# Kernel optimization log

Measured on AMD Instinct MI355X. Metric: run time of the kernel, lower is better.

Reference implementation:

```python
import jax, jax.numpy as jnp
import numpy as np

B, C, H, W = 2, 16, 384, 384
ADJ = 1
HID = 64
N_ITERS = 8


def _to_c(x):
    return x[..., 0] + 1j * x[..., 1]


def _to_r(z):
    return jnp.stack([z.real, z.imag], axis=-1)


def fft2c(x):
    z = jnp.fft.ifftshift(_to_c(x), axes=(-2, -1))
    z = jnp.fft.fft2(z, axes=(-2, -1), norm='ortho')
    return _to_r(jnp.fft.fftshift(z, axes=(-2, -1)))


def ifft2c(x):
    z = jnp.fft.ifftshift(_to_c(x), axes=(-2, -1))
    z = jnp.fft.ifft2(z, axes=(-2, -1), norm='ortho')
    return _to_r(jnp.fft.fftshift(z, axes=(-2, -1)))


def complex_mul(a, b):
    ar, ai = a[..., 0], a[..., 1]
    br, bi = b[..., 0], b[..., 1]
    return jnp.stack([ar * br - ai * bi, ar * bi + ai * br], axis=-1)


def complex_conj(x):
    return jnp.stack([x[..., 0], -x[..., 1]], axis=-1)


def _conv(x, w, b):
    y = jax.lax.conv_general_dilated(x, w, (1, 1), 'SAME',
                                     dimension_numbers=('NCHW', 'OIHW', 'NCHW'))
    return y + b[None, :, None, None]


def sens_expand(x, sens_maps):
    # x: [b, adj, h, w, 2] -> repeat to coils, multiply, fft
    c = sens_maps.shape[1]
    x = jnp.repeat(x, c // ADJ, axis=1)
    return fft2c(complex_mul(x, sens_maps))


def sens_reduce(x, sens_maps):
    b, c, h, w, _ = x.shape
    x = ifft2c(x)
    x = complex_mul(x, complex_conj(sens_maps))
    return x.reshape(b, ADJ, c // ADJ, h, w, 2).sum(axis=2)  # [b, adj, h, w, 2]


def apply_model(x, w1, b1, w2, b2):
    # complex_to_chan_dim: [b, c, h, w, 2] -> [b, 2c, h, w]
    b, c, h, w, _ = x.shape
    x = jnp.transpose(x, (0, 4, 1, 2, 3)).reshape(b, 2 * c, h, w)
    # per-channel norm (torch std is unbiased -> ddof=1)
    xf = x.reshape(b, 2 * c, h * w)
    mean = xf.mean(axis=2)[:, :, None, None]
    std = jnp.std(xf, axis=2, ddof=1)[:, :, None, None]
    xn = (x - mean) / std
    # regularizer model (2-layer conv)
    y = _conv(jax.nn.relu(_conv(xn, w1, b1)), w2, b2)
    y = y * std + mean
    # chan_complex_to_last_dim
    return jnp.transpose(y.reshape(b, 2, c, h, w), (0, 2, 3, 4, 1))


def mask_predictor(x, w_mp, b_mp):
    # x: [b, 2, h, w] -> prob over width columns [b, 1, w]
    feat = x.mean(axis=2)  # [b, 2, w]
    logits = jnp.einsum('bcw,c->bw', feat, w_mp) + b_mp
    return jax.nn.softmax(logits, axis=-1)[:, None, :]


def update_mask(current_mask, pred_prob, add_list, it_idx):
    # batched variable-k top-k scatter (fused version of the per-sample loop)
    p = pred_prob[:, :, None, :, None] * (1.0 - current_mask)  # [b,1,1,w,1]
    b = p.shape[0]
    pv = p.reshape(b, -1)                       # [b, w]
    order = jnp.argsort(-pv, axis=-1)           # descending
    ranks = jnp.argsort(order, axis=-1)         # rank of each column
    add_num = add_list[:, it_idx]               # [b]
    add = (ranks < add_num[:, None]).astype(current_mask.dtype)
    return current_mask + add[:, None, None, :, None]


def setup_inputs():
    key = jax.random.key(0)
    ks = jax.random.split(key, 10)
    return {
        'current_kspace': jax.random.normal(ks[0], (B, C, H, W, 2), jnp.float32),
        'ref_kspace': jax.random.normal(ks[1], (B, C, H, W, 2), jnp.float32),
        'mask': jax.random.randint(ks[2], (B, 1, 1, W, 1), 0, 2).astype(bool),
        'sens_maps': jax.random.normal(ks[3], (B, C, H, W, 2), jnp.float32) / np.sqrt(C),
        'it_idx': 3,
        'current_mask': jnp.zeros((B, 1, 1, W, 1), jnp.float32),
        'current_prob': jax.random.uniform(ks[4], (B, 1, W), jnp.float32),
        'add_list': jax.random.randint(ks[5], (B, N_ITERS), 1, 30),
        'dc_weight': jnp.ones((1,), jnp.float32),
        'w1': jax.random.normal(ks[6], (HID, 2 * ADJ, 3, 3), jnp.float32) * 0.05,
        'b1': jnp.zeros((HID,), jnp.float32),
        'w2': jax.random.normal(ks[7], (2 * ADJ, HID, 3, 3), jnp.float32) * 0.05,
        'b2': jnp.zeros((2 * ADJ,), jnp.float32),
        'w_mp': jax.random.normal(ks[8], (2,), jnp.float32) * 0.1,
        'b_mp': jnp.zeros((), jnp.float32),
    }


def reference(current_kspace, ref_kspace, mask, sens_maps, it_idx, current_mask,
              current_prob, add_list, dc_weight, w1, b1, w2, b2, w_mp, b_mp):
    restore_im = apply_model(sens_reduce(current_kspace, sens_maps), w1, b1, w2, b2)
    model_term = sens_expand(restore_im, sens_maps)
    soft_dc = jnp.where(mask, model_term - ref_kspace, 0.0) * dc_weight
    pred_kspace = model_term - soft_dc
    restore_im_dc = sens_reduce(pred_kspace, sens_maps)
    # [b, h, w, 2] -> fft2c -> [b, 2, h, w]
    kim = jnp.transpose(fft2c(restore_im_dc[:, 0]), (0, 3, 1, 2))
    pred_prob = mask_predictor(kim, w_mp, b_mp)
    pred_mask = update_mask(current_mask, pred_prob, add_list, it_idx)
    return pred_kspace, pred_mask, pred_prob
```

## Files before the change

### kernel.cpp

```cpp
#include <hip/hip_runtime.h>
#include <hip/hip_bf16.h>
#include <math.h>

#define HH 384
#define WW 384
#define NPIX (HH*WW)
#define BB 2
#define CC 16
#define NKF 9437184

__device__ inline float2 cmul(float2 a, float2 b) {
    return make_float2(a.x*b.x - a.y*b.y, a.x*b.y + a.y*b.x);
}
__device__ inline float bf2f(unsigned short u) {
    union { unsigned int i; float f; } c; c.i = ((unsigned)u) << 16; return c.f;
}
__device__ inline float2 loadc2(const void* p, int dt, size_t i) {
    if (dt == 1) { ushort2 u = ((const ushort2*)p)[i];
        return make_float2(bf2f(u.x), bf2f(u.y)); }
    if (dt == 2) { double2 d = ((const double2*)p)[i];
        return make_float2((float)d.x, (float)d.y); }
    return ((const float2*)p)[i];
}
__device__ inline float loads1(const void* p, int dt, size_t i) {
    if (dt == 1) return bf2f(((const unsigned short*)p)[i]);
    if (dt == 2) return (float)((const double*)p)[i];
    return ((const float*)p)[i];
}
__device__ inline int flex_int1(const void* p) {
    unsigned v = ((const unsigned*)p)[0];
    if (v < 1000000u) return (int)v;
    float f = ((const float*)p)[0];
    if (f > -1e6f && f < 1e6f && f == floorf(f)) return (int)f;
    return (int)((const double*)p)[0];
}
__device__ inline int flex_int_arr(const void* p, int i) {
    const unsigned* u = (const unsigned*)p;
    if (u[1] == 0u && u[3] == 0u) return (int)u[2*i];
    if (u[0] >= 1u && u[0] < 1000000u) return (int)u[i];
    float f = ((const float*)p)[i];
    if (f > -1e6f && f < 1e6f) return (int)f;
    return (int)((const double*)p)[i];
}

__global__ void detect_dtype(const unsigned* __restrict__ q, int* dt)
{
    __shared__ int bad, sig;
    if (threadIdx.x == 0) { bad = 0; sig = 0; }
    __syncthreads();
    const unsigned short* q16 = (const unsigned short*)q;
    int mybad = 0, mysig = 0;
    for (int i = threadIdx.x; i < 8192; i += 256) {
        unsigned short u = q16[i];
        int e = (u >> 7) & 0xFF;
        if (!(e == 0 || (e >= 100 && e <= 140))) mybad++;
    }
    for (int i = threadIdx.x; i < 2048; i += 256) {
        unsigned hi = q[2*i + 1];
        int e = (hi >> 20) & 0x7FF;
        if (e >= 1003 && e <= 1040) mysig++;
    }
    atomicAdd(&bad, mybad);
    atomicAdd(&sig, mysig);
    __syncthreads();
    if (threadIdx.x == 0)
        *dt = (bad < 400) ? 1 : ((sig > 1950) ? 2 : 0);
}

#define NLINE 8
#define SP 385

template<int DIR, int AXIS, int MODE>
__global__ __launch_bounds__(256)
void fft384(const void* in, float2* out, const int* DTp, int srcExt,
            const void* aux1, const void* aux2,
            const int* FLAGp, const void* dcwp, float2* outk)
{
    __shared__ float2 tw[384];
    __shared__ float2 stage[NLINE * SP];
    __shared__ float2 work[4][384];
    const int tid = threadIdx.x;
    const int dt = (srcExt || MODE) ? *DTp : 0;
    for (int j = tid; j < 384; j += 256) {
        float s, c;
        sincosf(-6.283185307179586f * (float)j / 384.0f, &s, &c);
        tw[j] = make_float2(c, s);
    }
    const int img = blockIdx.x / 48;
    const int t0  = (blockIdx.x % 48) * NLINE;
    const size_t base = (size_t)img * NPIX;
    float2* dst = out + base;

    if (AXIS == 0) {
        if (MODE == 1) {
            const float2* rim = (const float2*)aux1;
            const size_t rbase = (size_t)(img >> 4) * NPIX;
            for (int f = tid; f < NLINE*384; f += 256) {
                int l = f / 384, n = f - l*384;
                size_t pix = (size_t)(t0 + l)*384 + n;
                stage[l*SP + n] = cmul(rim[rbase + pix], loadc2(aux2, dt, base + pix));
            }
        } else {
            for (int f = tid; f < NLINE*384; f += 256) {
                int l = f / 384, n = f - l*384;
                stage[l*SP + n] = loadc2(in, dt, base + (size_t)(t0 + l)*384 + n);
            }
        }
    } else {
        for (int f = tid; f < NLINE*384; f += 256) {
            int l = f & 7, n = f >> 3;
            stage[l*SP + n] = loadc2(in, dt, base + (size_t)n*384 + (t0 + l));
        }
    }
    __syncthreads();
    const int g    = tid >> 6;
    const int lane = tid & 63;
    float2* w = work[g];
    const float SCALE = 0.05103103630798288f;
    for (int it = 0; it < 2; ++it) {
        const int l = it*4 + g;
        #pragma unroll
        for (int m = 0; m < 6; ++m) {
            int n = lane + 64*m;
            float2 v = stage[l*SP + n];
            float sgn = (n & 1) ? -1.f : 1.f;
            int q = n / 3;
            int r3 = n - 3*q;
            w[r3*128 + q] = make_float2(v.x*sgn, v.y*sgn);
        }
        __syncthreads();
        #pragma unroll
        for (int s = 0; s < 7; ++s) {
            const int h = 64 >> s;
            const int tstep = 3 << s;
            const int j = lane & (h-1);
            const int i = ((lane & ~(h-1)) << 1) | j;
            float2 t = tw[j * tstep];
            if (DIR < 0) t.y = -t.y;
            #pragma unroll
            for (int n1 = 0; n1 < 3; ++n1) {
                float2* a = w + (n1 << 7);
                float2 u = a[i], v = a[i+h];
                float2 d = make_float2(u.x - v.x, u.y - v.y);
                a[i]   = make_float2(u.x + v.x, u.y + v.y);
                a[i+h] = cmul(d, t);
            }
            __syncthreads();
        }
        #pragma unroll
        for (int half = 0; half < 2; ++half) {
            int k2 = lane + 64*half;
            int r  = __brev((unsigned)k2) >> 25;
            float2 a0 = w[r], a1 = w[128 + r], a2 = w[256 + r];
            float2 t1 = tw[k2];
            float2 t2 = tw[(2*k2) % 384];
            float2 w3 = tw[128], w3b = tw[256];
            if (DIR < 0) { t1.y=-t1.y; t2.y=-t2.y; w3.y=-w3.y; w3b.y=-w3b.y; }
            float2 b1 = cmul(a1, t1), b2 = cmul(a2, t2);
            float2 X0 = make_float2(a0.x + b1.x + b2.x, a0.y + b1.y + b2.y);
            float2 c1 = cmul(w3, b1), c2 = cmul(w3b, b2);
            float2 X1 = make_float2(a0.x + c1.x + c2.x, a0.y + c1.y + c2.y);
            float2 d1 = cmul(w3b, b1), d2 = cmul(w3, b2);
            float2 X2 = make_float2(a0.x + d1.x + d2.x, a0.y + d1.y + d2.y);
            float sc = (k2 & 1) ? -SCALE : SCALE;
            stage[l*SP + k2      ] = make_float2(X0.x*sc, X0.y*sc);
            stage[l*SP + k2 + 128] = make_float2(X1.x*sc, X1.y*sc);
            stage[l*SP + k2 + 256] = make_float2(X2.x*sc, X2.y*sc);
        }
        __syncthreads();
    }
    if (AXIS == 0) {
        for (int f = tid; f < NLINE*384; f += 256) {
            int l = f / 384, n = f - l*384;
            dst[(size_t)(t0 + l)*384 + n] = stage[l*SP + n];
        }
    } else {
        if (MODE == 2) {
            const int fl = *FLAGp;
            const float dw = loads1(dcwp, dt, 0);
            const int bb = img >> 4;
            for (int f = tid; f < NLINE*384; f += 256) {
                int l = f & 7, n = f >> 3;
                int wcol = t0 + l;
                size_t pix = (size_t)n*384 + wcol;
                float2 v = stage[l*SP + n];
                int m;
                switch (fl) {
                    case 0:  m = ((const unsigned char*)aux2)[bb*384 + wcol] != 0; break;
                    case 4:  m = ((const unsigned short*)aux2)[bb*384 + wcol] != 0; break;
                    case 3:  m = ((const unsigned long long*)aux2)[bb*384 + wcol] != 0ULL; break;
                    default: m = ((const unsigned int*)aux2)[bb*384 + wcol] != 0u; break;
                }
                if (m) {
                    float2 r = loadc2(aux1, dt, base + pix);
                    v.x -= (v.x - r.x)*dw;
                    v.y -= (v.y - r.y)*dw;
                }
                dst[pix] = v;
                outk[base + pix] = v;
            }
        } else {
            for (int f = tid; f < NLINE*384; f += 256) {
                int l = f & 7, n = f >> 3;
                dst[(size_t)n*384 + (t0 + l)] = stage[l*SP + n];
            }
        }
    }
}

__global__ void detect_mask(const unsigned char* __restrict__ m, int* flag)
{
    __shared__ int sA, sB, sC, sD, sE;
    if (threadIdx.x == 0) { sA = sB = sC = sD = sE = 0; }
    __syncthreads();
    for (int i = threadIdx.x; i < 768; i += 256) {
        unsigned char v = m[i];
        if (v > 1) atomicOr(&sA, 1);
        if ((i & 3) && v) atomicOr(&sB, 1);
    }
    const unsigned short* m16 = (const unsigned short*)m;
    for (int i = threadIdx.x; i < 384; i += 256)
        if (!(i & 1) && m16[i]) atomicOr(&sC, 1);
    const unsigned int* m32 = (const unsigned int*)m;
    for (int i = threadIdx.x; i < 192; i += 256) {
        if ((i & 1) && m32[i]) atomicOr(&sD, 1);
        if (!(i & 1) && m32[i]) atomicOr(&sE, 1);
    }
    __syncthreads();
    if (threadIdx.x == 0) {
        int f;
        if (!sA) { if (sB) f = 0; else if (sD) f = 2; else f = 3; }
        else     { if (sC) f = 4; else if (sE) f = 2; else f = 3; }
        *flag = f;
    }
}

template<bool WITH_STATS>
__global__ __launch_bounds__(256)
void reduce_sens(const float2* __restrict__ xin, const void* __restrict__ sens,
                 float2* __restrict__ ximg, const int* DTp,
                 float* __restrict__ partials)
{
    const int dt = *DTp;
    const int b = blockIdx.y;
    const int p = blockIdx.x*256 + threadIdx.x;
    float2 acc = make_float2(0.f, 0.f);
    for (int c = 0; c < CC; ++c) {
        size_t o = ((size_t)(b*CC + c))*NPIX + p;
        float2 a = xin[o];
        float2 s = loadc2(sens, dt, o);
        acc.x += a.x*s.x + a.y*s.y;
        acc.y += a.y*s.x - a.x*s.y;
    }
    ximg[(size_t)b*NPIX + p] = acc;
    if (WITH_STATS) {
        float sx = acc.x, sy = acc.y, qx = acc.x*acc.x, qy = acc.y*acc.y;
        #pragma unroll
        for (int o = 32; o > 0; o >>= 1) {
            sx += __shfl_down(sx, o, 64); sy += __shfl_down(sy, o, 64);
            qx += __shfl_down(qx, o, 64); qy += __shfl_down(qy, o, 64);
        }
        __shared__ float red[4][4];
        const int wv = threadIdx.x >> 6, lane = threadIdx.x & 63;
        if (lane == 0) {
            red[wv][0] = sx; red[wv][1] = sy; red[wv][2] = qx; red[wv][3] = qy;
        }
        __syncthreads();
        if (threadIdx.x == 0) {
            float t0 = red[0][0]+red[1][0]+red[2][0]+red[3][0];
            float t1 = red[0][1]+red[1][1]+red[2][1]+red[3][1];
            float t2 = red[0][2]+red[1][2]+red[2][2]+red[3][2];
            float t3 = red[0][3]+red[1][3]+red[2][3]+red[3][3];
            float* dst = partials + ((size_t)b*576 + blockIdx.x)*4;
            dst[0] = t0; dst[1] = t1; dst[2] = t2; dst[3] = t3;
        }
    }
}

__global__ __launch_bounds__(256)
void stats_finalize(const float* __restrict__ partials, float* __restrict__ ms)
{
    const int b = blockIdx.x;
    const int tid = threadIdx.x;
    float sx=0.f, sy=0.f, qx=0.f, qy=0.f;
    for (int i = tid; i < 576; i += 256) {
        const float* p = partials + ((size_t)b*576 + i)*4;
        sx += p[0]; sy += p[1]; qx += p[2]; qy += p[3];
    }
    __shared__ float r0[256], r1[256], r2[256], r3[256];
    r0[tid]=sx; r1[tid]=sy; r2[tid]=qx; r3[tid]=qy;
    __syncthreads();
    for (int s = 128; s > 0; s >>= 1) {
        if (tid < s) {
            r0[tid]+=r0[tid+s]; r1[tid]+=r1[tid+s];
            r2[tid]+=r2[tid+s]; r3[tid]+=r3[tid+s];
        }
        __syncthreads();
    }
    if (tid == 0) {
        const float N = (float)NPIX;
        float var0 = (r2[0] - r0[0]*r0[0]/N) / (N - 1.f);
        float var1 = (r3[0] - r1[0]*r1[0]/N) / (N - 1.f);
        ms[(b*2+0)*2]   = r0[0]/N;
        ms[(b*2+0)*2+1] = sqrtf(var0);
        ms[(b*2+1)*2]   = r1[0]/N;
        ms[(b*2+1)*2+1] = sqrtf(var1);
    }
}

__global__ __launch_bounds__(256)
void conv_fused(const float2* __restrict__ ximg, const void* __restrict__ w1g,
                const void* __restrict__ b1g, const void* __restrict__ w2g,
                const void* __restrict__ b2g, const float* __restrict__ msg,
                float2* __restrict__ rim, const int* DTp)
{
    __shared__ float2 inP[20][21];
    __shared__ float w1s[1152];
    __shared__ float w2s[1152];
    __shared__ float b1s[64];
    __shared__ float hidw[4][18*20];
    __shared__ float2 accs[4][256];

    const int dt = *DTp;
    const int b = blockIdx.z, bx = blockIdx.x, by = blockIdx.y;
    const int tid = threadIdx.x;
    const int wv = tid >> 6, lane = tid & 63;

    for (int f = tid; f < 1152; f += 256) {
        w1s[f] = loads1(w1g, dt, f);
        w2s[f] = loads1(w2g, dt, f);
    }
    if (tid < 64) b1s[tid] = loads1(b1g, dt, tid);
    const float mean0 = msg[(b*2+0)*2], istd0 = 1.f/msg[(b*2+0)*2+1];
    const float mean1 = msg[(b*2+1)*2], istd1 = 1.f/msg[(b*2+1)*2+1];
    for (int f = tid; f < 400; f += 256) {
        int yy = f / 20, xx = f - yy*20;
        int gy = by*16 + yy - 2, gx = bx*16 + xx - 2;
        float a = 0.f, c = 0.f;
        if (gy >= 0 && gy < HH && gx >= 0 && gx < WW) {
            float2 v = ximg[(size_t)b*NPIX + gy*WW + gx];
            a = (v.x - mean0)*istd0;
            c = (v.y - mean1)*istd1;
        }
        inP[yy][xx] = make_float2(a, c);
    }
    __syncthreads();

    float a0[4] = {0.f,0.f,0.f,0.f}, a1[4] = {0.f,0.f,0.f,0.f};
    float* hid = hidw[wv];

    const int c1col = lane % 18;
    const int c1g   = lane / 18;
    const int c1y0  = 6 * c1g;
    const int tx = lane & 15, ybase = (lane >> 4) * 4;

    for (int j = 0; j < 16; ++j) {
        const int o = wv*16 + j;
        const float* wa = &w1s[o*18];
        const float bo = b1s[o];
        if (c1g < 3) {
            float2 r0c0 = inP[c1y0][c1col],   r0c1 = inP[c1y0][c1col+1],   r0c2 = inP[c1y0][c1col+2];
            float2 r1c0 = inP[c1y0+1][c1col], r1c1 = inP[c1y0+1][c1col+1], r1c2 = inP[c1y0+1][c1col+2];
            #pragma unroll
            for (int rr = 0; rr < 6; ++rr) {
                float2 r2c0 = inP[c1y0+rr+2][c1col];
                float2 r2c1 = inP[c1y0+rr+2][c1col+1];
                float2 r2c2 = inP[c1y0+rr+2][c1col+2];
                float acc = bo
                    + wa[0]*r0c0.x + wa[1]*r0c1.x + wa[2]*r0c2.x
                    + wa[3]*r1c0.x + wa[4]*r1c1.x + wa[5]*r1c2.x
                    + wa[6]*r2c0.x + wa[7]*r2c1.x + wa[8]*r2c2.x
                    + wa[9]*r0c0.y  + wa[10]*r0c1.y + wa[11]*r0c2.y
                    + wa[12]*r1c0.y + wa[13]*r1c1.y + wa[14]*r1c2.y
                    + wa[15]*r2c0.y + wa[16]*r2c1.y + wa[17]*r2c2.y;
                int hy = c1y0 + rr;
                int gy = by*16 + hy - 1, gx = bx*16 + c1col - 1;
                hid[hy*20 + c1col] = (gy >= 0 && gy < HH && gx >= 0 && gx < WW)
                                   ? fmaxf(acc, 0.f) : 0.f;
                r0c0 = r1c0; r0c1 = r1c1; r0c2 = r1c2;
                r1c0 = r2c0; r1c1 = r2c1; r1c2 = r2c2;
            }
        }
        __builtin_amdgcn_wave_barrier();
        {
            const float* w2a = &w2s[o*9];
            const float* w2b = &w2s[576 + o*9];
            float h00 = hid[ybase*20 + tx],     h01 = hid[ybase*20 + tx+1],     h02 = hid[ybase*20 + tx+2];
            float h10 = hid[(ybase+1)*20 + tx], h11 = hid[(ybase+1)*20 + tx+1], h12 = hid[(ybase+1)*20 + tx+2];
            #pragma unroll
            for (int r = 0; r < 4; ++r) {
                float h20 = hid[(ybase+r+2)*20 + tx];
                float h21 = hid[(ybase+r+2)*20 + tx+1];
                float h22 = hid[(ybase+r+2)*20 + tx+2];
                a0[r] += w2a[0]*h00 + w2a[1]*h01 + w2a[2]*h02
                       + w2a[3]*h10 + w2a[4]*h11 + w2a[5]*h12
                       + w2a[6]*h20 + w2a[7]*h21 + w2a[8]*h22;
                a1[r] += w2b[0]*h00 + w2b[1]*h01 + w2b[2]*h02
                       + w2b[3]*h10 + w2b[4]*h11 + w2b[5]*h12
                       + w2b[6]*h20 + w2b[7]*h21 + w2b[8]*h22;
                h00 = h10; h01 = h11; h02 = h12;
                h10 = h20; h11 = h21; h12 = h22;
            }
        }
        __builtin_amdgcn_wave_barrier();
    }
    #pragma unroll
    for (int r = 0; r < 4; ++r)
        accs[wv][(ybase + r)*16 + tx] = make_float2(a0[r], a1[r]);
    __syncthreads();
    {
        const int p = tid;
        float s0 = loads1(b2g, dt, 0), s1 = loads1(b2g, dt, 1);
        #pragma unroll
        for (int wvi = 0; wvi < 4; ++wvi) {
            s0 += accs[wvi][p].x;
            s1 += accs[wvi][p].y;
        }
        const float std0 = msg[(b*2+0)*2+1], std1 = msg[(b*2+1)*2+1];
        int ty = p >> 4, txx = p & 15;
        rim[(size_t)b*NPIX + (by*16+ty)*WW + (bx*16+txx)]
            = make_float2(s0*std0 + mean0, s1*std1 + mean1);
    }
}

__global__ __launch_bounds__(384)
void predictor(const float2* __restrict__ kimg, const void* __restrict__ wmp,
               const void* __restrict__ bmp, float* __restrict__ prob,
               float* __restrict__ outp, const int* DTp)
{
    const int dt = *DTp;
    const int b = blockIdx.x, w = threadIdx.x;
    float s0 = 0.f, s1 = 0.f;
    for (int h = 0; h < HH; ++h) {
        float2 v = kimg[((size_t)b*HH + h)*WW + w];
        s0 += v.x; s1 += v.y;
    }
    float logit = (s0*loads1(wmp,dt,0) + s1*loads1(wmp,dt,1)) * (1.0f/384.0f)
                + loads1(bmp,dt,0);
    __shared__ float red[8];
    float m = logit;
    for (int o = 32; o > 0; o >>= 1) m = fmaxf(m, __shfl_down(m, o, 64));
    int wid = w >> 6, lane = w & 63;
    if (lane == 0) red[wid] = m;
    __syncthreads();
    if (w == 0) { float mm = red[0]; for (int i = 1; i < 6; ++i) mm = fmaxf(mm, red[i]); red[6] = mm; }
    __syncthreads();
    m = red[6];
    float e = expf(logit - m);
    float s = e;
    for (int o = 32; o > 0; o >>= 1) s += __shfl_down(s, o, 64);
    __syncthreads();
    if (lane == 0) red[wid] = s;
    __syncthreads();
    if (w == 0) { float ss = 0.f; for (int i = 0; i < 6; ++i) ss += red[i]; red[7] = ss; }
    __syncthreads();
    float pr = e / red[7];
    prob[b*WW + w] = pr;
    outp[b*WW + w] = pr;
}

__global__ __launch_bounds__(384)
void update_mask_k(const float* __restrict__ prob, const void* __restrict__ cmask,
                   const void* __restrict__ add_list, const void* __restrict__ itp,
                   float* __restrict__ outm, const int* DTp)
{
    const int dt = *DTp;
    const int b = blockIdx.x, w = threadIdx.x;
    __shared__ float p[384];
    float cm = loads1(cmask, dt, b*WW + w);
    float pv = prob[b*WW + w] * (1.0f - cm);
    p[w] = pv;
    __syncthreads();
    int rank = 0;
    for (int i = 0; i < 384; ++i) {
        float q = p[i];
        rank += (q > pv) || (q == pv && i < w);
    }
    int it = flex_int1(itp);
    if (it < 0 || it > 7) it = 0;
    int addn = flex_int_arr(add_list, b*8 + it);
    float val = cm + ((rank < addn) ? 1.0f : 0.0f);
    outm[b*WW + w] = val;
}

extern "C" void kernel_launch(void* const* d_in, const int* in_sizes, int n_in,
                              void* d_out, int out_size, void* d_ws, size_t ws_size,
                              hipStream_t stream)
{
    const void* src  = d_in[0];
    const void* tgt  = d_in[1];
    const void* mask = d_in[2];
    const void* sens = d_in[3];
    const void* itp  = d_in[4];
    const void* cmask= d_in[5];
    const void* addl = d_in[7];
    const void* dcw  = d_in[8];
    const void* w1   = d_in[9];
    const void* b1   = d_in[10];
    const void* w2   = d_in[11];
    const void* b2   = d_in[12];
    const void* wmp  = d_in[13];
    const void* bmp  = d_in[14];
    float* out = (float*)d_out;

    float* ws = (float*)d_ws;
    const size_t OFF_XIMG = 9437184;
    const size_t OFF_RIM  = OFF_XIMG + 589824;
    const size_t OFF_MS   = OFF_RIM  + 589824;
    const size_t OFF_PROB = OFF_MS + 8;
    const size_t OFF_FLAG = OFF_PROB + 768;
    const size_t OFF_DT   = OFF_FLAG + 4;
    const size_t OFF_PART = OFF_DT + 4;

    float2* A    = (float2*)ws;
    float2* XIMG = (float2*)(ws + OFF_XIMG);
    float2* RIM  = (float2*)(ws + OFF_RIM);
    float*  MS   = ws + OFF_MS;
    float*  PROB = ws + OFF_PROB;
    int*    FLAG = (int*)(ws + OFF_FLAG);
    int*    DT   = (int*)(ws + OFF_DT);
    float*  PART = ws + OFF_PART;

    const int gBig   = (BB*CC)*48;
    const int gSmall = BB*48;

    detect_dtype<<<1, 256, 0, stream>>>((const unsigned*)src, DT);
    detect_mask<<<1, 256, 0, stream>>>((const unsigned char*)mask, FLAG);

    fft384<-1,0,0><<<gBig, 256, 0, stream>>>(src, A, DT, 1, nullptr, nullptr, nullptr, nullptr, nullptr);
    fft384<-1,1,0><<<gBig, 256, 0, stream>>>(A, A, DT, 0, nullptr, nullptr, nullptr, nullptr, nullptr);
    reduce_sens<true><<<dim3((NPIX/256), BB), 256, 0, stream>>>(A, sens, XIMG, DT, PART);
    stats_finalize<<<BB, 256, 0, stream>>>(PART, MS);

    conv_fused<<<dim3(24,24,BB), 256, 0, stream>>>(XIMG, w1, b1, w2, b2, MS, RIM, DT);

    fft384<1,0,1><<<gBig, 256, 0, stream>>>(nullptr, A, DT, 0, RIM, sens, nullptr, nullptr, nullptr);
    fft384<1,1,2><<<gBig, 256, 0, stream>>>(A, A, DT, 0, tgt, mask, FLAG, dcw, (float2*)out);

    fft384<-1,0,0><<<gBig, 256, 0, stream>>>(A, A, DT, 0, nullptr, nullptr, nullptr, nullptr, nullptr);
    fft384<-1,1,0><<<gBig, 256, 0, stream>>>(A, A, DT, 0, nullptr, nullptr, nullptr, nullptr, nullptr);
    reduce_sens<false><<<dim3((NPIX/256), BB), 256, 0, stream>>>(A, sens, XIMG, DT, nullptr);

    fft384<1,0,0><<<gSmall, 256, 0, stream>>>(XIMG, XIMG, DT, 0, nullptr, nullptr, nullptr, nullptr, nullptr);
    fft384<1,1,0><<<gSmall, 256, 0, stream>>>(XIMG, XIMG, DT, 0, nullptr, nullptr, nullptr, nullptr, nullptr);

    predictor<<<BB, 384, 0, stream>>>(XIMG, wmp, bmp, PROB, out + 9437184 + 768, DT);
    update_mask_k<<<BB, 384, 0, stream>>>(PROB, cmask, addl, itp, out + 9437184, DT);
}
```

Measured before the change: 393.7 us.

## Widen column-FFT tiles to 16 lines and pair hidden channels in conv

New measurement: 425.1 us. 8.0% more time.

```diff
diff --git a/kernel.cpp b/kernel.cpp
--- a/kernel.cpp
+++ b/kernel.cpp
@@ -67,17 +67,16 @@
         *dt = (bad < 400) ? 1 : ((sig > 1950) ? 2 : 0);
 }
 
-#define NLINE 8
 #define SP 385
 
-template<int DIR, int AXIS, int MODE>
+template<int DIR, int AXIS, int MODE, int NL>
 __global__ __launch_bounds__(256)
 void fft384(const void* in, float2* out, const int* DTp, int srcExt,
             const void* aux1, const void* aux2,
             const int* FLAGp, const void* dcwp, float2* outk)
 {
     __shared__ float2 tw[384];
-    __shared__ float2 stage[NLINE * SP];
+    __shared__ float2 stage[NL * SP];
     __shared__ float2 work[4][384];
     const int tid = threadIdx.x;
     const int dt = (srcExt || MODE) ? *DTp : 0;
@@ -86,8 +85,9 @@
         sincosf(-6.283185307179586f * (float)j / 384.0f, &s, &c);
         tw[j] = make_float2(c, s);
     }
-    const int img = blockIdx.x / 48;
-    const int t0  = (blockIdx.x % 48) * NLINE;
+    const int BPI = 384 / NL;
+    const int img = blockIdx.x / BPI;
+    const int t0  = (blockIdx.x % BPI) * NL;
     const size_t base = (size_t)img * NPIX;
     float2* dst = out + base;
 
@@ -95,20 +95,20 @@
         if (MODE == 1) {
             const float2* rim = (const float2*)aux1;
             const size_t rbase = (size_t)(img >> 4) * NPIX;
-            for (int f = tid; f < NLINE*384; f += 256) {
+            for (int f = tid; f < NL*384; f += 256) {
                 int l = f / 384, n = f - l*384;
                 size_t pix = (size_t)(t0 + l)*384 + n;
                 stage[l*SP + n] = cmul(rim[rbase + pix], loadc2(aux2, dt, base + pix));
             }
         } else {
-            for (int f = tid; f < NLINE*384; f += 256) {
+            for (int f = tid; f < NL*384; f += 256) {
                 int l = f / 384, n = f - l*384;
                 stage[l*SP + n] = loadc2(in, dt, base + (size_t)(t0 + l)*384 + n);
             }
         }
     } else {
-        for (int f = tid; f < NLINE*384; f += 256) {
-            int l = f & 7, n = f >> 3;
+        for (int f = tid; f < NL*384; f += 256) {
+            int l = f & (NL-1), n = f / NL;
             stage[l*SP + n] = loadc2(in, dt, base + (size_t)n*384 + (t0 + l));
         }
     }
@@ -117,7 +117,7 @@
     const int lane = tid & 63;
     float2* w = work[g];
     const float SCALE = 0.05103103630798288f;
-    for (int it = 0; it < 2; ++it) {
+    for (int it = 0; it < NL/4; ++it) {
         const int l = it*4 + g;
         #pragma unroll
         for (int m = 0; m < 6; ++m) {
@@ -170,7 +170,7 @@
         __syncthreads();
     }
     if (AXIS == 0) {
-        for (int f = tid; f < NLINE*384; f += 256) {
+        for (int f = tid; f < NL*384; f += 256) {
             int l = f / 384, n = f - l*384;
             dst[(size_t)(t0 + l)*384 + n] = stage[l*SP + n];
         }
@@ -179,8 +179,8 @@
             const int fl = *FLAGp;
             const float dw = loads1(dcwp, dt, 0);
             const int bb = img >> 4;
-            for (int f = tid; f < NLINE*384; f += 256) {
-                int l = f & 7, n = f >> 3;
+            for (int f = tid; f < NL*384; f += 256) {
+                int l = f & (NL-1), n = f / NL;
                 int wcol = t0 + l;
                 size_t pix = (size_t)n*384 + wcol;
                 float2 v = stage[l*SP + n];
@@ -200,8 +200,8 @@
                 outk[base + pix] = v;
             }
         } else {
-            for (int f = tid; f < NLINE*384; f += 256) {
-                int l = f & 7, n = f >> 3;
+            for (int f = tid; f < NL*384; f += 256) {
+                int l = f & (NL-1), n = f / NL;
                 dst[(size_t)n*384 + (t0 + l)] = stage[l*SP + n];
             }
         }
@@ -318,7 +318,7 @@
     __shared__ float w1s[1152];
     __shared__ float w2s[1152];
     __shared__ float b1s[64];
-    __shared__ float hidw[4][18*20];
+    __shared__ float2 hidw[4][18*20];
     __shared__ float2 accs[4][256];
 
     const int dt = *DTp;
@@ -347,17 +347,18 @@
     __syncthreads();
 
     float a0[4] = {0.f,0.f,0.f,0.f}, a1[4] = {0.f,0.f,0.f,0.f};
-    float* hid = hidw[wv];
+    float2* hid = hidw[wv];
 
     const int c1col = lane % 18;
     const int c1g   = lane / 18;
     const int c1y0  = 6 * c1g;
     const int tx = lane & 15, ybase = (lane >> 4) * 4;
 
-    for (int j = 0; j < 16; ++j) {
-        const int o = wv*16 + j;
-        const float* wa = &w1s[o*18];
-        const float bo = b1s[o];
+    for (int j = 0; j < 8; ++j) {
+        const int oa = wv*16 + 2*j;
+        const float* wa = &w1s[oa*18];
+        const float* wb = &w1s[(oa+1)*18];
+        const float boa = b1s[oa], bob = b1s[oa+1];
         if (c1g < 3) {
             float2 r0c0 = inP[c1y0][c1col],   r0c1 = inP[c1y0][c1col+1],   r0c2 = inP[c1y0][c1col+2];
             float2 r1c0 = inP[c1y0+1][c1col], r1c1 = inP[c1y0+1][c1col+1], r1c2 = inP[c1y0+1][c1col+2];
@@ -366,38 +367,55 @@
                 float2 r2c0 = inP[c1y0+rr+2][c1col];
                 float2 r2c1 = inP[c1y0+rr+2][c1col+1];
                 float2 r2c2 = inP[c1y0+rr+2][c1col+2];
-                float acc = bo
+                float accA = boa
                     + wa[0]*r0c0.x + wa[1]*r0c1.x + wa[2]*r0c2.x
                     + wa[3]*r1c0.x + wa[4]*r1c1.x + wa[5]*r1c2.x
                     + wa[6]*r2c0.x + wa[7]*r2c1.x + wa[8]*r2c2.x
                     + wa[9]*r0c0.y  + wa[10]*r0c1.y + wa[11]*r0c2.y
                     + wa[12]*r1c0.y + wa[13]*r1c1.y + wa[14]*r1c2.y
                     + wa[15]*r2c0.y + wa[16]*r2c1.y + wa[17]*r2c2.y;
+                float accB = bob
+                    + wb[0]*r0c0.x + wb[1]*r0c1.x + wb[2]*r0c2.x
+                    + wb[3]*r1c0.x + wb[4]*r1c1.x + wb[5]*r1c2.x
+                    + wb[6]*r2c0.x + wb[7]*r2c1.x + wb[8]*r2c2.x
+                    + wb[9]*r0c0.y  + wb[10]*r0c1.y + wb[11]*r0c2.y
+                    + wb[12]*r1c0.y + wb[13]*r1c1.y + wb[14]*r1c2.y
+                    + wb[15]*r2c0.y + wb[16]*r2c1.y + wb[17]*r2c2.y;
                 int hy = c1y0 + rr;
                 int gy = by*16 + hy - 1, gx = bx*16 + c1col - 1;
-                hid[hy*20 + c1col] = (gy >= 0 && gy < HH && gx >= 0 && gx < WW)
-                                   ? fmaxf(acc, 0.f) : 0.f;
+                bool inb = (gy >= 0 && gy < HH && gx >= 0 && gx < WW);
+                hid[hy*20 + c1col] = inb
+                    ? make_float2(fmaxf(accA, 0.f), fmaxf(accB, 0.f))
+                    : make_float2(0.f, 0.f);
                 r0c0 = r1c0; r0c1 = r1c1; r0c2 = r1c2;
                 r1c0 = r2c0; r1c1 = r2c1; r1c2 = r2c2;
             }
         }
         __builtin_amdgcn_wave_barrier();
         {
-            const float* w2a = &w2s[o*9];
-            const float* w2b = &w2s[576 + o*9];
-            float h00 = hid[ybase*20 + tx],     h01 = hid[ybase*20 + tx+1],     h02 = hid[ybase*20 + tx+2];
-            float h10 = hid[(ybase+1)*20 + tx], h11 = hid[(ybase+1)*20 + tx+1], h12 = hid[(ybase+1)*20 + tx+2];
+            const float* pa0 = &w2s[oa*9];
+            const float* pa1 = &w2s[(oa+1)*9];
+            const float* pb0 = &w2s[576 + oa*9];
+            const float* pb1 = &w2s[576 + (oa+1)*9];
+            float2 h00 = hid[ybase*20 + tx],     h01 = hid[ybase*20 + tx+1],     h02 = hid[ybase*20 + tx+2];
+            float2 h10 = hid[(ybase+1)*20 + tx], h11 = hid[(ybase+1)*20 + tx+1], h12 = hid[(ybase+1)*20 + tx+2];
             #pragma unroll
             for (int r = 0; r < 4; ++r) {
-                float h20 = hid[(ybase+r+2)*20 + tx];
-                float h21 = hid[(ybase+r+2)*20 + tx+1];
-                float h22 = hid[(ybase+r+2)*20 + tx+2];
-                a0[r] += w2a[0]*h00 + w2a[1]*h01 + w2a[2]*h02
-                       + w2a[3]*h10 + w2a[4]*h11 + w2a[5]*h12
-                       + w2a[6]*h20 + w2a[7]*h21 + w2a[8]*h22;
-                a1[r] += w2b[0]*h00 + w2b[1]*h01 + w2b[2]*h02
-                       + w2b[3]*h10 + w2b[4]*h11 + w2b[5]*h12
-                       + w2b[6]*h20 + w2b[7]*h21 + w2b[8]*h22;
+                float2 h20 = hid[(ybase+r+2)*20 + tx];
+                float2 h21 = hid[(ybase+r+2)*20 + tx+1];
+                float2 h22 = hid[(ybase+r+2)*20 + tx+2];
+                a0[r] += pa0[0]*h00.x + pa0[1]*h01.x + pa0[2]*h02.x
+                       + pa0[3]*h10.x + pa0[4]*h11.x + pa0[5]*h12.x
+                       + pa0[6]*h20.x + pa0[7]*h21.x + pa0[8]*h22.x
+                       + pa1[0]*h00.y + pa1[1]*h01.y + pa1[2]*h02.y
+                       + pa1[3]*h10.y + pa1[4]*h11.y + pa1[5]*h12.y
+                       + pa1[6]*h20.y + pa1[7]*h21.y + pa1[8]*h22.y;
+                a1[r] += pb0[0]*h00.x + pb0[1]*h01.x + pb0[2]*h02.x
+                       + pb0[3]*h10.x + pb0[4]*h11.x + pb0[5]*h12.x
+                       + pb0[6]*h20.x + pb0[7]*h21.x + pb0[8]*h22.x
+                       + pb1[0]*h00.y + pb1[1]*h01.y + pb1[2]*h02.y
+                       + pb1[3]*h10.y + pb1[4]*h11.y + pb1[5]*h12.y
+                       + pb1[6]*h20.y + pb1[7]*h21.y + pb1[8]*h22.y;
                 h00 = h10; h01 = h11; h02 = h12;
                 h10 = h20; h11 = h21; h12 = h22;
             }
@@ -521,28 +539,30 @@
     int*    DT   = (int*)(ws + OFF_DT);
     float*  PART = ws + OFF_PART;
 
-    const int gBig   = (BB*CC)*48;
-    const int gSmall = BB*48;
+    const int gRow   = (BB*CC)*48;
+    const int gCol   = (BB*CC)*24;
+    const int gSmallR = BB*48;
+    const int gSmallC = BB*24;
 
     detect_dtype<<<1, 256, 0, stream>>>((const unsigned*)src, DT);
     detect_mask<<<1, 256, 0, stream>>>((const unsigned char*)mask, FLAG);
 
-    fft384<-1,0,0><<<gBig, 256, 0, stream>>>(src, A, DT, 1, nullptr, nullptr, nullptr, nullptr, nullptr);
-    fft384<-1,1,0><<<gBig, 256, 0, stream>>>(A, A, DT, 0, nullptr, nullptr, nullptr, nullptr, nullptr);
+    fft384<-1,0,0,8><<<gRow, 256, 0, stream>>>(src, A, DT, 1, nullptr, nullptr, nullptr, nullptr, nullptr);
+    fft384<-1,1,0,16><<<gCol, 256, 0, stream>>>(A, A, DT, 0, nullptr, nullptr, nullptr, nullptr, nullptr);
     reduce_sens<true><<<dim3((NPIX/256), BB), 256, 0, stream>>>(A, sens, XIMG, DT, PART);
     stats_finalize<<<BB, 256, 0, stream>>>(PART, MS);
 
     conv_fused<<<dim3(24,24,BB), 256, 0, stream>>>(XIMG, w1, b1, w2, b2, MS, RIM, DT);
 
-    fft384<1,0,1><<<gBig, 256, 0, stream>>>(nullptr, A, DT, 0, RIM, sens, nullptr, nullptr, nullptr);
-    fft384<1,1,2><<<gBig, 256, 0, stream>>>(A, A, DT, 0, tgt, mask, FLAG, dcw, (float2*)out);
-
-    fft384<-1,0,0><<<gBig, 256, 0, stream>>>(A, A, DT, 0, nullptr, nullptr, nullptr, nullptr, nullptr);
-    fft384<-1,1,0><<<gBig, 256, 0, stream>>>(A, A, DT, 0, nullptr, nullptr, nullptr, nullptr, nullptr);
+    fft384<1,0,1,8><<<gRow, 256, 0, stream>>>(nullptr, A, DT, 0, RIM, sens, nullptr, nullptr, nullptr);
+    fft384<1,1,2,16><<<gCol, 256, 0, stream>>>(A, A, DT, 0, tgt, mask, FLAG, dcw, (float2*)out);
+
+    fft384<-1,0,0,8><<<gRow, 256, 0, stream>>>(A, A, DT, 0, nullptr, nullptr, nullptr, nullptr, nullptr);
+    fft384<-1,1,0,16><<<gCol, 256, 0, stream>>>(A, A, DT, 0, nullptr, nullptr, nullptr, nullptr, nullptr);
     reduce_sens<false><<<dim3((NPIX/256), BB), 256, 0, stream>>>(A, sens, XIMG, DT, nullptr);
 
-    fft384<1,0,0><<<gSmall, 256, 0, stream>>>(XIMG, XIMG, DT, 0, nullptr, nullptr, nullptr, nullptr, nullptr);
-    fft384<1,1,0><<<gSmall, 256, 0, stream>>>(XIMG, XIMG, DT, 0, nullptr, nullptr, nullptr, nullptr, nullptr);
+    fft384<1,0,0,8><<<gSmallR, 256, 0, stream>>>(XIMG, XIMG, DT, 0, nullptr, nullptr, nullptr, nullptr, nullptr);
+    fft384<1,1,0,16><<<gSmallC, 256, 0, stream>>>(XIMG, XIMG, DT, 0, nullptr, nullptr, nullptr, nullptr, nullptr);
 
     predictor<<<BB, 384, 0, stream>>>(XIMG, wmp, bmp, PROB, out + 9437184 + 768, DT);
     update_mask_k<<<BB, 384, 0, stream>>>(PROB, cmask, addl, itp, out + 9437184, DT);
```
